# Optimization experiments

Measured on AMD Instinct MI355X. Metric: run time of the kernel, lower is better.

## Reference

```python
import jax, jax.numpy as jnp
from jax import lax
import numpy as np

# (pad, pool_kernel(h,w), pool_stride(h,w)) for each of the 7 conv layers
_CONV_CFG = [
    (1, (2, 2), (2, 2)),
    (1, (2, 2), (2, 2)),
    (1, (2, 2), (2, 1)),
    (1, (2, 2), (2, 1)),
    (1, (2, 2), (2, 2)),
    (1, (2, 2), (2, 1)),
    (0, (1, 1), (1, 1)),
]


def _conv_layer(x, w, b, pad, pool_k, pool_s):
    y = lax.conv_general_dilated(x, w, (1, 1), [(pad, pad), (pad, pad)],
                                 dimension_numbers=("NCHW", "OIHW", "NCHW"))
    y = jax.nn.relu(y + b[None, :, None, None])
    if pool_k != (1, 1):
        y = lax.reduce_window(y, -jnp.inf, lax.max, (1, 1) + pool_k, (1, 1) + pool_s, "VALID")
    return y


def _lstm_dir(x, wih, whh, bih, bhh, reverse):
    # x: [B,T,I]; PyTorch gate order i,f,g,o
    B = x.shape[0]
    H = whh.shape[1]
    xg = jnp.einsum("bti,gi->btg", x, wih) + bih + bhh  # [B,T,4H]

    def step(carry, xt):
        h, c = carry
        g = xt + h @ whh.T
        i, f, gg, o = jnp.split(g, 4, axis=-1)
        c = jax.nn.sigmoid(f) * c + jax.nn.sigmoid(i) * jnp.tanh(gg)
        h = jax.nn.sigmoid(o) * jnp.tanh(c)
        return (h, c), h

    init = (jnp.zeros((B, H), x.dtype), jnp.zeros((B, H), x.dtype))
    _, hs = lax.scan(step, init, jnp.swapaxes(xg, 0, 1), reverse=reverse)
    return jnp.swapaxes(hs, 0, 1)  # [B,T,H], time-ordered for both directions


def _bilstm2(x, wih, whh, bih, bhh, base):
    # 2-layer bidirectional LSTM; weight slots base..base+3 = (l0_fwd,l0_bwd,l1_fwd,l1_bwd)
    for l in range(2):
        i0 = base + 2 * l
        fwd = _lstm_dir(x, wih[i0], whh[i0], bih[i0], bhh[i0], False)
        bwd = _lstm_dir(x, wih[i0 + 1], whh[i0 + 1], bih[i0 + 1], bhh[i0 + 1], True)
        x = jnp.concatenate([fwd, bwd], axis=-1)
    return x


def _forward(x, conv_w0, conv_b0, conv_w1, conv_b1, conv_w2, conv_b2, conv_w3, conv_b3,
             conv_w4, conv_b4, conv_w5, conv_b5, conv_w6, conv_b6,
             lstm_wih, lstm_whh, lstm_bih, lstm_bhh,
             enc_proj_w, enc_proj_b, dec_proj_w, dec_proj_b, v_w,
             dec_wih, dec_whh, dec_bih, dec_bhh, dense_w, dense_b):
    conv_w = [conv_w0, conv_w1, conv_w2, conv_w3, conv_w4, conv_w5, conv_w6]
    conv_b = [conv_b0, conv_b1, conv_b2, conv_b3, conv_b4, conv_b5, conv_b6]
    y = x
    for i, (pad, pk, ps) in enumerate(_CONV_CFG):
        y = _conv_layer(y, conv_w[i], conv_b[i], pad, pk, ps)
    # y: [B,512,1,T] -> squeeze height, put time first-major: [B,T,512]
    y = jnp.transpose(y[:, :, 0, :], (0, 2, 1))
    seq = _bilstm2(y, lstm_wih, lstm_whh, lstm_bih, lstm_bhh, 0)
    seq = _bilstm2(seq, lstm_wih, lstm_whh, lstm_bih, lstm_bhh, 4)  # [B,T,512]

    # additive attention: enc projection is h-independent, precompute once
    enc = jnp.einsum("bte,ae->bta", seq, enc_proj_w) + enc_proj_b  # [B,T,256]
    B = x.shape[0]

    def dec_step(carry, _):
        h, c = carry
        dec = h @ dec_proj_w.T + dec_proj_b                      # [B,256]
        scores = jnp.tanh(enc + dec[:, None, :]) @ v_w[0]        # [B,T]
        aw = jax.nn.softmax(scores, axis=1)
        ctx = jnp.einsum("bt,bte->be", aw, seq)                  # [B,512]
        g = ctx @ dec_wih.T + dec_bih + h @ dec_whh.T + dec_bhh  # [B,2048]
        i, f, gg, o = jnp.split(g, 4, axis=-1)
        c = jax.nn.sigmoid(f) * c + jax.nn.sigmoid(i) * jnp.tanh(gg)
        h = jax.nn.sigmoid(o) * jnp.tanh(c)
        return (h, c), h @ dense_w.T + dense_b

    init = (jnp.zeros((B, 512), x.dtype), jnp.zeros((B, 512), x.dtype))
    _, outs = lax.scan(dec_step, init, None, length=25)  # [25,B,99] == permute(1,0,2)
    return outs


def setup_inputs() -> dict:
    key = jax.random.key(0)
    ks = jax.random.split(key, 32)

    def rn(i, shape, std):
        return jax.random.normal(ks[i], shape, jnp.float32) * std

    d = {"x": jax.random.normal(ks[0], (16, 1, 128, 512), jnp.float32)}
    chans = [(1, 64, 3), (64, 128, 3), (128, 256, 3), (256, 512, 3),
             (512, 512, 3), (512, 512, 3), (512, 512, 2)]
    for i, (ci, co, k) in enumerate(chans):
        d[f"conv_w{i}"] = rn(1 + i, (co, ci, k, k), (2.0 / (ci * k * k)) ** 0.5)
        d[f"conv_b{i}"] = rn(8 + i, (co,), 0.02)
    d["lstm_wih"] = rn(15, (8, 1024, 512), 0.06)
    d["lstm_whh"] = rn(16, (8, 1024, 256), 0.06)
    d["lstm_bih"] = rn(17, (8, 1024), 0.06)
    d["lstm_bhh"] = rn(18, (8, 1024), 0.06)
    d["enc_proj_w"] = rn(19, (256, 512), 0.04)
    d["enc_proj_b"] = rn(20, (256,), 0.02)
    d["dec_proj_w"] = rn(21, (256, 512), 0.04)
    d["dec_proj_b"] = rn(22, (256,), 0.02)
    d["v_w"] = rn(23, (1, 256), 0.06)
    d["dec_wih"] = rn(24, (2048, 512), 0.04)
    d["dec_whh"] = rn(25, (2048, 512), 0.04)
    d["dec_bih"] = rn(26, (2048,), 0.02)
    d["dec_bhh"] = rn(27, (2048,), 0.02)
    d["dense_w"] = rn(28, (99, 512), 0.04)
    d["dense_b"] = rn(29, (99,), 0.02)
    return d


def reference(x, conv_w0, conv_b0, conv_w1, conv_b1, conv_w2, conv_b2, conv_w3, conv_b3,
              conv_w4, conv_b4, conv_w5, conv_b5, conv_w6, conv_b6,
              lstm_wih, lstm_whh, lstm_bih, lstm_bhh,
              enc_proj_w, enc_proj_b, dec_proj_w, dec_proj_b, v_w,
              dec_wih, dec_whh, dec_bih, dec_bhh, dense_w, dense_b):
    return _forward(x, conv_w0, conv_b0, conv_w1, conv_b1, conv_w2, conv_b2, conv_w3, conv_b3,
                    conv_w4, conv_b4, conv_w5, conv_b5, conv_w6, conv_b6,
                    lstm_wih, lstm_whh, lstm_bih, lstm_bhh,
                    enc_proj_w, enc_proj_b, dec_proj_w, dec_proj_b, v_w,
                    dec_wih, dec_whh, dec_bih, dec_bhh, dense_w, dense_b)
```

## Files before the change

kernel.cpp:

```cpp
#include <hip/hip_runtime.h>
#include <math.h>

typedef short bf16x8 __attribute__((ext_vector_type(8)));
typedef short s16x4  __attribute__((ext_vector_type(4)));
typedef float f32x4  __attribute__((ext_vector_type(4)));

__device__ __forceinline__ float sigmf(float x){ return 1.f/(1.f+expf(-x)); }
__device__ __forceinline__ short f2bf(float f){
    unsigned u = __float_as_uint(f);
    u = (u + 0x7FFFu + ((u>>16)&1u)) >> 16;
    return (short)u;
}
__device__ __forceinline__ float bf2f(short s){
    return __uint_as_float(((unsigned)(unsigned short)s) << 16);
}

__global__ void wsplit(const float* __restrict__ w, short* __restrict__ whi, short* __restrict__ wlo,
                       int Cout, int Cin, int KW, int total)
{
    int idx = blockIdx.x*256 + threadIdx.x;
    if (idx >= total) return;
    int l = idx & 63; int t = idx >> 6;
    int KST = Cin >> 5;
    int ks = t % KST; t /= KST;
    int nCoQ = Cout >> 4;
    int coQ = t % nCoQ; int kk = t / nCoQ;
    int ky = kk / KW, kx = kk % KW;
    int co = coQ*16 + (l & 15);
    int ci = ks*32 + (l >> 4)*8;
    bf16x8 h, lo;
#pragma unroll
    for (int e = 0; e < 8; ++e) {
        float wv = w[(((size_t)co*Cin + ci + e)*KW + ky)*KW + kx];
        short hb = f2bf(wv);
        h[e] = hb;
        lo[e] = f2bf(wv - bf2f(hb));
    }
    ((bf16x8*)whi)[idx] = h;
    ((bf16x8*)wlo)[idx] = lo;
}

__global__ void wsplit_g(const float* __restrict__ w, short* __restrict__ out)
{
    int slot = blockIdx.y;
    int i = blockIdx.x*256 + threadIdx.x;
    int l = i & 63, t = i >> 6;
    int kc = t & 15, nQ = t >> 4;
    int n = nQ*16 + (l & 15);
    int k = kc*32 + (l >> 4)*8;
    const float* src = w + ((size_t)slot*1024 + n)*512 + k;
    bf16x8 h, lo;
#pragma unroll
    for (int e = 0; e < 8; ++e) {
        float wv = src[e];
        short hb = f2bf(wv);
        h[e] = hb;
        lo[e] = f2bf(wv - bf2f(hb));
    }
    short* o = out + (size_t)slot*1048576;
    ((bf16x8*)o)[i] = h;
    ((bf16x8*)(o + 524288))[i] = lo;
}

template<int KW, int PKH, int PKW, int PSW, int PAD, bool FUSE0>
__launch_bounds__(256)
__global__ void conv_mfma(const float* __restrict__ in, const short* __restrict__ wm,
                          const float* __restrict__ bias, float* __restrict__ out,
                          int Cin, int H, int W, int Cout, int Hp, int Wp, int Wel,
                          const float* __restrict__ w0, const float* __restrict__ b0)
{
    constexpr int TAPS = KW*KW;
    constexpr int SR   = PKH + KW - 1;
    constexpr int XT   = 64;
    constexpr int XTH  = 67;
    constexpr int POB  = (XT - PKW)/PSW + 1;
    __shared__ union {
        short s[2][16][XTH][8];
        float y[64][132];
    } u;
    __shared__ float w0s[640];

    const int tid  = threadIdx.x;
    const int lane = tid & 63;
    const int wid  = tid >> 6;
    const int l15  = lane & 15, l4 = lane >> 4;
    const int nCoT = Cout >> 7;
    const int b    = blockIdx.z / nCoT;
    const int ct   = blockIdx.z % nCoT;
    const int co_blk = ct << 7;
    const int hp   = blockIdx.y;
    const int px0  = blockIdx.x * POB;
    const int x0   = px0 * PSW;
    const int y0   = hp * PKH;
    const int cow  = wid >> 1;
    const int xw   = (wid & 1) * 32;
    const int KST  = Cin >> 5;
    const int nCoQ = Cout >> 4;

    if constexpr (FUSE0) {
        for (int i = tid; i < 640; i += 256) w0s[i] = (i < 576) ? w0[i] : b0[i-576];
    }

    f32x4 acc[4][2][PKH];
#pragma unroll
    for (int c = 0; c < 4; ++c)
#pragma unroll
        for (int xf = 0; xf < 2; ++xf)
#pragma unroll
            for (int r = 0; r < PKH; ++r) acc[c][xf][r] = (f32x4){0.f,0.f,0.f,0.f};

    const float* inb = FUSE0 ? (in + (size_t)b*128*512) : (in + (size_t)b*H*W*Cin);

    for (int ci0 = 0; ci0 < Cin; ci0 += 32) {
        __syncthreads();
        constexpr int ITEMS = SR*XTH*4;
        for (int it = tid; it < ITEMS; it += 256) {
            int kslot = it & 3;
            int x  = (it >> 2) % XTH;
            int r  = (it >> 2) / XTH;
            int y  = y0 - PAD + r;
            int xg = x0 - PAD + x;
            float v[8];
            if constexpr (FUSE0) {
                if (y >= 0 && y < H && xg >= 0 && xg < W) {
                    float xin[4][4];
                    int iy0 = 2*y - 1, ix0 = 2*xg - 1;
#pragma unroll
                    for (int dy = 0; dy < 4; ++dy) {
                        int iy = iy0 + dy;
                        bool oky = (iy >= 0) && (iy < 128);
#pragma unroll
                        for (int dx = 0; dx < 4; ++dx) {
                            int ix = ix0 + dx;
                            xin[dy][dx] = (oky && ix >= 0 && ix < 512) ? inb[(size_t)iy*512 + ix] : 0.f;
                        }
                    }
#pragma unroll
                    for (int c = 0; c < 8; ++c) {
                        int co = ci0 + kslot*8 + c;
                        const float* w9 = &w0s[co*9];
                        float p00=0.f,p01=0.f,p10=0.f,p11=0.f;
#pragma unroll
                        for (int ky = 0; ky < 3; ++ky)
#pragma unroll
                            for (int kx = 0; kx < 3; ++kx) {
                                float wv = w9[ky*3+kx];
                                p00 = fmaf(xin[ky  ][kx  ], wv, p00);
                                p01 = fmaf(xin[ky  ][kx+1], wv, p01);
                                p10 = fmaf(xin[ky+1][kx  ], wv, p10);
                                p11 = fmaf(xin[ky+1][kx+1], wv, p11);
                            }
                        float m = fmaxf(fmaxf(p00,p01), fmaxf(p10,p11)) + w0s[576+co];
                        v[c] = fmaxf(m, 0.f);
                    }
                } else {
#pragma unroll
                    for (int c = 0; c < 8; ++c) v[c] = 0.f;
                }
            } else {
                if (y >= 0 && y < H && xg >= 0 && xg < W) {
                    const float* p = inb + ((size_t)y*W + xg)*Cin + ci0 + kslot*8;
                    float4 a = *(const float4*)p;
                    float4 bq = *(const float4*)(p+4);
                    v[0]=a.x; v[1]=a.y; v[2]=a.z; v[3]=a.w;
                    v[4]=bq.x; v[5]=bq.y; v[6]=bq.z; v[7]=bq.w;
                } else {
#pragma unroll
                    for (int c = 0; c < 8; ++c) v[c] = 0.f;
                }
            }
            bf16x8 h8, l8;
#pragma unroll
            for (int c = 0; c < 8; ++c) {
                short hb = f2bf(v[c]);
                h8[c] = hb;
                l8[c] = f2bf(v[c] - bf2f(hb));
            }
            *(bf16x8*)&u.s[0][r*4+kslot][x][0] = h8;
            *(bf16x8*)&u.s[1][r*4+kslot][x][0] = l8;
        }
        __syncthreads();

        const int ks = ci0 >> 5;
        for (int kk = 0; kk < TAPS; ++kk) {
            const int ky = kk / KW, kx = kk % KW;
            bf16x8 ah[4], al[4];
            const size_t abase = (((size_t)kk*nCoQ + (co_blk>>4) + cow*4)*KST + ks)*512 + lane*8;
            const size_t cstr  = (size_t)KST*512;
#pragma unroll
            for (int c = 0; c < 4; ++c) {
                ah[c] = *(const bf16x8*)(wm + abase + c*cstr);
                al[c] = *(const bf16x8*)(wm + Wel + abase + c*cstr);
            }
#pragma unroll
            for (int r = 0; r < PKH; ++r) {
                const int sr = r + ky;
                bf16x8 bh[2], bl[2];
#pragma unroll
                for (int xf = 0; xf < 2; ++xf) {
                    int xcol = xw + xf*16 + l15 + kx;
                    bh[xf] = *(const bf16x8*)&u.s[0][sr*4 + l4][xcol][0];
                    bl[xf] = *(const bf16x8*)&u.s[1][sr*4 + l4][xcol][0];
                }
#pragma unroll
                for (int c = 0; c < 4; ++c)
#pragma unroll
                    for (int xf = 0; xf < 2; ++xf) {
                        acc[c][xf][r] = __builtin_amdgcn_mfma_f32_16x16x32_bf16(ah[c], bh[xf], acc[c][xf][r], 0,0,0);
                        acc[c][xf][r] = __builtin_amdgcn_mfma_f32_16x16x32_bf16(ah[c], bl[xf], acc[c][xf][r], 0,0,0);
                        acc[c][xf][r] = __builtin_amdgcn_mfma_f32_16x16x32_bf16(al[c], bh[xf], acc[c][xf][r], 0,0,0);
                    }
            }
        }
    }

    __syncthreads();
#pragma unroll
    for (int c = 0; c < 4; ++c) {
        int co_l = cow*64 + c*16 + l4*4;
        float4 b4 = *(const float4*)&bias[co_blk + co_l];
#pragma unroll
        for (int xf = 0; xf < 2; ++xf) {
            f32x4 v = acc[c][xf][0];
            if (PKH == 2) {
                f32x4 v1 = acc[c][xf][1];
                v[0]=fmaxf(v[0],v1[0]); v[1]=fmaxf(v[1],v1[1]);
                v[2]=fmaxf(v[2],v1[2]); v[3]=fmaxf(v[3],v1[3]);
            }
            v[0]+=b4.x; v[1]+=b4.y; v[2]+=b4.z; v[3]+=b4.w;
            int x = xw + xf*16 + l15;
            *(f32x4*)&u.y[x][co_l] = v;
        }
    }
    __syncthreads();
    for (int i = tid; i < POB*128; i += 256) {
        int co = i & 127, p = i >> 7;
        int x = p * PSW;
        float v = u.y[x][co];
        if (PKW == 2) v = fmaxf(v, u.y[x+1][co]);
        v = fmaxf(v, 0.f);
        int px = px0 + p;
        if (px < Wp)
            out[(((size_t)b*Hp + hp)*Wp + px)*Cout + co_blk + co] = v;
    }
}

__launch_bounds__(256)
__global__ void gemm_mfma(const float* __restrict__ A, const short* __restrict__ wg,
                          const float* __restrict__ bi, const float* __restrict__ bh,
                          float* __restrict__ Cf, float* __restrict__ Cb,
                          int M, int s0)
{
    __shared__ short sa[2][4][64][8];
    const int tid = threadIdx.x;
    const int lane = tid & 63;
    const int wid = tid >> 6;
    const int l15 = lane & 15, l4 = lane >> 4;
    const int cow = wid >> 1;
    const int xw  = wid & 1;
    const int m0 = blockIdx.x * 64;
    const int n0 = blockIdx.y * 128;
    const int slot = s0 + blockIdx.z;
    const short* whi = wg + (size_t)slot * 1048576;
    const short* wlo = whi + 524288;
    float* C = blockIdx.z ? Cb : Cf;
    const float* b1 = bi + slot*1024;
    const float* b2 = bh + slot*1024;

    const int mg  = wid;
    const int pos = tid & 63;
    const int sm  = mg*16 + (pos & 15);
    const int skl = pos >> 4;
    const int gm  = m0 + sm;
    const int nQb = blockIdx.y*8 + cow*4;

    f32x4 acc[4][2];
#pragma unroll
    for (int c = 0; c < 4; ++c)
#pragma unroll
        for (int xf = 0; xf < 2; ++xf) acc[c][xf] = (f32x4){0.f,0.f,0.f,0.f};

    for (int kc = 0; kc < 16; ++kc) {
        __syncthreads();
        {
            float v[8];
            if (gm < M) {
                const float* ap = A + (size_t)gm*512 + kc*32 + skl*8;
                float4 q0 = *(const float4*)ap;
                float4 q1 = *(const float4*)(ap+4);
                v[0]=q0.x; v[1]=q0.y; v[2]=q0.z; v[3]=q0.w;
                v[4]=q1.x; v[5]=q1.y; v[6]=q1.z; v[7]=q1.w;
            } else {
#pragma unroll
                for (int e = 0; e < 8; ++e) v[e] = 0.f;
            }
            bf16x8 h8, l8;
#pragma unroll
            for (int e = 0; e < 8; ++e) {
                short hb = f2bf(v[e]);
                h8[e] = hb;
                l8[e] = f2bf(v[e] - bf2f(hb));
            }
            *(bf16x8*)&sa[0][mg][pos][0] = h8;
            *(bf16x8*)&sa[1][mg][pos][0] = l8;
        }
        __syncthreads();

        bf16x8 ah[4], al[4];
#pragma unroll
        for (int c = 0; c < 4; ++c) {
            size_t off = (((size_t)(nQb + c)*16 + kc)*64 + lane)*8;
            ah[c] = *(const bf16x8*)(whi + off);
            al[c] = *(const bf16x8*)(wlo + off);
        }
        bf16x8 bhv[2], blv[2];
#pragma unroll
        for (int xf = 0; xf < 2; ++xf) {
            bhv[xf] = *(const bf16x8*)&sa[0][xw*2+xf][lane][0];
            blv[xf] = *(const bf16x8*)&sa[1][xw*2+xf][lane][0];
        }
#pragma unroll
        for (int c = 0; c < 4; ++c)
#pragma unroll
            for (int xf = 0; xf < 2; ++xf) {
                acc[c][xf] = __builtin_amdgcn_mfma_f32_16x16x32_bf16(ah[c], bhv[xf], acc[c][xf], 0,0,0);
                acc[c][xf] = __builtin_amdgcn_mfma_f32_16x16x32_bf16(ah[c], blv[xf], acc[c][xf], 0,0,0);
                acc[c][xf] = __builtin_amdgcn_mfma_f32_16x16x32_bf16(al[c], bhv[xf], acc[c][xf], 0,0,0);
            }
    }

#pragma unroll
    for (int c = 0; c < 4; ++c) {
        int n = n0 + cow*64 + c*16 + l4*4;
        float4 bb1 = *(const float4*)&b1[n];
        float4 bb2 = *(const float4*)&b2[n];
#pragma unroll
        for (int xf = 0; xf < 2; ++xf) {
            int m = m0 + xw*32 + xf*16 + l15;
            if (m < M) {
                f32x4 a = acc[c][xf];
                float4 o;
                o.x = a[0] + bb1.x + bb2.x;
                o.y = a[1] + bb1.y + bb2.y;
                o.z = a[2] + bb1.z + bb2.z;
                o.w = a[3] + bb1.w + bb2.w;
                *(float4*)&C[(size_t)m*1024 + n] = o;
            }
        }
    }
}

__launch_bounds__(256)
__global__ void gemm_nt(const float* __restrict__ A, const float* __restrict__ Bm,
                        const float* __restrict__ bias1, const float* __restrict__ bias2,
                        float* __restrict__ C, int M, int N, int K)
{
    __shared__ float As[16][68];
    __shared__ float Bs[16][68];
    const int tid = threadIdx.x;
    const int tx = tid & 15, ty = tid >> 4;
    const int row0 = blockIdx.y*64, col0 = blockIdx.x*64;
    float acc[4][4] = {};
    for (int k0 = 0; k0 < K; k0 += 16) {
#pragma unroll
        for (int i = 0; i < 4; ++i) {
            int e  = tid + i*256;
            int r  = e >> 4, kk = e & 15;
            int gr = row0 + r, gk = k0 + kk;
            As[kk][r] = (gr < M) ? A[(size_t)gr*K + gk] : 0.f;
            int gc = col0 + r;
            Bs[kk][r] = (gc < N) ? Bm[(size_t)gc*K + gk] : 0.f;
        }
        __syncthreads();
#pragma unroll
        for (int kk = 0; kk < 16; ++kk) {
            float av[4], bv[4];
#pragma unroll
            for (int i=0;i<4;++i) av[i] = As[kk][ty*4+i];
#pragma unroll
            for (int j=0;j<4;++j) bv[j] = Bs[kk][tx*4+j];
#pragma unroll
            for (int i=0;i<4;++i)
#pragma unroll
                for (int j=0;j<4;++j) acc[i][j] = fmaf(av[i], bv[j], acc[i][j]);
        }
        __syncthreads();
    }
#pragma unroll
    for (int i=0;i<4;++i)
#pragma unroll
        for (int j=0;j<4;++j) {
            int r = row0 + ty*4 + i, cc = col0 + tx*4 + j;
            if (r < M && cc < N) {
                float v = acc[i][j];
                if (bias1) v += bias1[cc];
                if (bias2) v += bias2[cc];
                C[(size_t)r*N + cc] = v;
            }
        }
}

__global__ void transpose2d(const float* __restrict__ in, float* __restrict__ out, int R, int C)
{
    int idx = blockIdx.x*256 + threadIdx.x;
    if (idx >= R*C) return;
    int r = idx / C, c = idx % C;
    out[(size_t)c*R + r] = in[idx];
}

__global__ void pack_whh_bf16(const float* __restrict__ in, short* __restrict__ out)
{
    int idx = blockIdx.x*256 + threadIdx.x;
    if (idx >= 8*1024*256) return;
    int l = idx / 262144, rem = idx % 262144;
    int g = rem >> 8, k = rem & 255;
    int j = g & 255, gate = g >> 8;
    out[(size_t)l*262144 + ((size_t)k*256 + j)*4 + gate] = f2bf(in[idx]);
}

__global__ void transpose_w4(const float* __restrict__ in, float* __restrict__ out)
{
    int idx = blockIdx.x*256 + threadIdx.x;
    if (idx >= 2048*512) return;
    int row = idx >> 9, k = idx & 511;
    int gate = row >> 9, j = row & 511;
    out[((size_t)k*512 + j)*4 + gate] = in[idx];
}

__launch_bounds__(1024)
__global__ void lstm_scan3(const float* __restrict__ xgf, const float* __restrict__ xgb,
                           const short* __restrict__ wBf, const short* __restrict__ wBb,
                           float* __restrict__ hout, int T)
{
    __shared__ float hs[256];
    __shared__ float part[4][256][4];
    const int b = blockIdx.x, dir = blockIdx.y;
    const int tid = threadIdx.x;
    const int j = tid & 255, ks = tid >> 8;
    const float* xg = dir ? xgb : xgf;
    const s16x4* w4 = (const s16x4*)(dir ? wBb : wBf);
    float c = 0.f;
    if (ks == 0) hs[j] = 0.f;
    __syncthreads();
    float* outp = hout + dir*256 + j;
    for (int s = 0; s < T; ++s) {
        int t = dir ? (T-1-s) : s;
        float xi=0.f, xf_=0.f, xg_=0.f, xo=0.f;
        if (ks == 0) {
            const float* xr = xg + ((size_t)b*T + t)*1024;
            xi = xr[j]; xf_ = xr[256+j]; xg_ = xr[512+j]; xo = xr[768+j];
        }
        float a0=0.f,a1=0.f,a2=0.f,a3=0.f;
        const s16x4* wp = w4 + (size_t)(ks*64)*256 + j;
#pragma unroll 16
        for (int kk = 0; kk < 64; ++kk) {
            float hv = hs[ks*64 + kk];
            s16x4 w = wp[(size_t)kk*256];
            a0 = fmaf(hv, bf2f(w[0]), a0);
            a1 = fmaf(hv, bf2f(w[1]), a1);
            a2 = fmaf(hv, bf2f(w[2]), a2);
            a3 = fmaf(hv, bf2f(w[3]), a3);
        }
        part[ks][j][0]=a0; part[ks][j][1]=a1; part[ks][j][2]=a2; part[ks][j][3]=a3;
        __syncthreads();
        if (ks == 0) {
            float gi = xi  + part[0][j][0]+part[1][j][0]+part[2][j][0]+part[3][j][0];
            float gf = xf_ + part[0][j][1]+part[1][j][1]+part[2][j][1]+part[3][j][1];
            float gg = xg_ + part[0][j][2]+part[1][j][2]+part[2][j][2]+part[3][j][2];
            float go = xo  + part[0][j][3]+part[1][j][3]+part[2][j][3]+part[3][j][3];
            c = sigmf(gf)*c + sigmf(gi)*tanhf(gg);
            float h = sigmf(go)*tanhf(c);
            hs[j] = h;
            outp[((size_t)b*T + t)*512] = h;
        }
        __syncthreads();
    }
}

__global__ void zero_hc(float* __restrict__ h, float* __restrict__ c)
{
    int i = blockIdx.x*256 + threadIdx.x;
    if (i < 16*512) { h[i] = 0.f; c[i] = 0.f; }
}

__launch_bounds__(256)
__global__ void dec_att(const float* __restrict__ h, const float* __restrict__ seq,
                        const float* __restrict__ enc, const float* __restrict__ dpwT,
                        const float* __restrict__ dpb, const float* __restrict__ vw,
                        float* __restrict__ ctx, int T)
{
    __shared__ float hsm[512], dec[256], sc[64];
    const int b = blockIdx.x, tid = threadIdx.x;
    hsm[tid]     = h[b*512 + tid];
    hsm[256+tid] = h[b*512 + 256 + tid];
    __syncthreads();
    float s = dpb[tid];
    for (int k = 0; k < 512; ++k) s = fmaf(hsm[k], dpwT[(size_t)k*256 + tid], s);
    dec[tid] = s;
    __syncthreads();
    {
        int t = tid >> 2, sub = tid & 3;
        float p = 0.f;
        if (t < T) {
            const float* er = enc + ((size_t)b*T + t)*256 + sub*64;
            const float* dc = dec + sub*64;
            const float* vv = vw + sub*64;
            for (int a = 0; a < 64; ++a) p = fmaf(tanhf(er[a] + dc[a]), vv[a], p);
        }
        p += __shfl_xor(p, 1, 4); p += __shfl_xor(p, 2, 4);
        if (t < T && sub == 0) sc[t] = p;
    }
    __syncthreads();
    if (tid < 64) {
        float v = (tid < T) ? sc[tid] : -1e30f;
        float m = v;
        for (int o = 1; o < 64; o <<= 1) m = fmaxf(m, __shfl_xor(m, o, 64));
        float e = (tid < T) ? expf(v - m) : 0.f;
        float ssum = e;
        for (int o = 1; o < 64; o <<= 1) ssum += __shfl_xor(ssum, o, 64);
        if (tid < T) sc[tid] = e / ssum;
    }
    __syncthreads();
#pragma unroll
    for (int half = 0; half < 2; ++half) {
        int col = tid + half*256;
        float acc = 0.f;
        const float* sr = seq + (size_t)b*T*512 + col;
        for (int t = 0; t < T; ++t) acc = fmaf(sc[t], sr[(size_t)t*512], acc);
        ctx[b*512 + col] = acc;
    }
}

__launch_bounds__(256)
__global__ void gates_part(const float* __restrict__ ctx, const float* __restrict__ h,
                           const float* __restrict__ wi4, const float* __restrict__ wh4,
                           float* __restrict__ gpart)
{
    __shared__ float xs[16][128], hsh[16][128];
    const int jt = blockIdx.x, ks = blockIdx.y;
    const int tid = threadIdx.x;
    const int jl = tid & 127, bh = tid >> 7;
    const int j = jt*128 + jl;
    const int k0 = ks*128;
    for (int idx = tid; idx < 2048; idx += 256) {
        int bb = idx >> 7, kk = idx & 127;
        xs[bb][kk]  = ctx[bb*512 + k0 + kk];
        hsh[bb][kk] = h[bb*512 + k0 + kk];
    }
    __syncthreads();
    float acc[8][4];
#pragma unroll
    for (int bi=0;bi<8;++bi)
#pragma unroll
        for (int g=0;g<4;++g) acc[bi][g]=0.f;
    const float4* wip = (const float4*)wi4 + (size_t)k0*512 + j;
    const float4* whp = (const float4*)wh4 + (size_t)k0*512 + j;
#pragma unroll 2
    for (int kk = 0; kk < 128; ++kk) {
        float4 wa = wip[(size_t)kk*512];
        float4 wb = whp[(size_t)kk*512];
#pragma unroll
        for (int bi = 0; bi < 8; ++bi) {
            int bb = bh*8 + bi;
            float xv = xs[bb][kk], hv = hsh[bb][kk];
            acc[bi][0] = fmaf(xv, wa.x, fmaf(hv, wb.x, acc[bi][0]));
            acc[bi][1] = fmaf(xv, wa.y, fmaf(hv, wb.y, acc[bi][1]));
            acc[bi][2] = fmaf(xv, wa.z, fmaf(hv, wb.z, acc[bi][2]));
            acc[bi][3] = fmaf(xv, wa.w, fmaf(hv, wb.w, acc[bi][3]));
        }
    }
    float* gp = gpart + (size_t)ks*16*2048;
#pragma unroll
    for (int bi = 0; bi < 8; ++bi)
#pragma unroll
        for (int g = 0; g < 4; ++g)
            gp[(size_t)(bh*8+bi)*2048 + j*4 + g] = acc[bi][g];
}

__launch_bounds__(512)
__global__ void cell_dense(float* __restrict__ h, float* __restrict__ c,
                           const float* __restrict__ gpart,
                           const float* __restrict__ bih, const float* __restrict__ bhh,
                           const float* __restrict__ dwT, const float* __restrict__ dnb,
                           float* __restrict__ out)
{
    __shared__ float hsh[512];
    const int b = blockIdx.x, j = threadIdx.x;
    float gi = bih[j]        + bhh[j];
    float gf = bih[512+j]    + bhh[512+j];
    float gg = bih[1024+j]   + bhh[1024+j];
    float go = bih[1536+j]   + bhh[1536+j];
#pragma unroll
    for (int ks = 0; ks < 4; ++ks) {
        float4 gp = *(const float4*)(gpart + (size_t)ks*16*2048 + (size_t)b*2048 + j*4);
        gi += gp.x; gf += gp.y; gg += gp.z; go += gp.w;
    }
    float cn = sigmf(gf)*c[b*512+j] + sigmf(gi)*tanhf(gg);
    float hn = sigmf(go)*tanhf(cn);
    c[b*512+j] = cn; h[b*512+j] = hn; hsh[j] = hn;
    __syncthreads();
    int o = j >> 2, sub = j & 3;
    float p = 0.f;
    if (o < 99) {
        const float* hk = hsh + sub*128;
        const float* wk = dwT + (size_t)sub*128*99 + o;
        for (int k = 0; k < 128; ++k) p = fmaf(hk[k], wk[(size_t)k*99], p);
    }
    p += __shfl_xor(p, 1, 4); p += __shfl_xor(p, 2, 4);
    if (o < 99 && sub == 0) out[b*99 + o] = p + dnb[o];
}

extern "C" void kernel_launch(void* const* d_in, const int* in_sizes, int n_in,
                              void* d_out, int out_size, void* d_ws, size_t ws_size,
                              hipStream_t stream)
{
    (void)in_sizes; (void)n_in; (void)out_size; (void)ws_size;
    const float* x = (const float*)d_in[0];
    const float* convw[7]; const float* convb[7];
    for (int i = 0; i < 7; ++i) { convw[i] = (const float*)d_in[1+2*i]; convb[i] = (const float*)d_in[2+2*i]; }
    const float* lw   = (const float*)d_in[15];
    const float* lr   = (const float*)d_in[16];
    const float* lbi  = (const float*)d_in[17];
    const float* lbh  = (const float*)d_in[18];
    const float* encW = (const float*)d_in[19];
    const float* encB = (const float*)d_in[20];
    const float* dpw  = (const float*)d_in[21];
    const float* dpb  = (const float*)d_in[22];
    const float* vw   = (const float*)d_in[23];
    const float* dwih = (const float*)d_in[24];
    const float* dwhh = (const float*)d_in[25];
    const float* dbih = (const float*)d_in[26];
    const float* dbhh = (const float*)d_in[27];
    const float* dnw  = (const float*)d_in[28];
    const float* dnb  = (const float*)d_in[29];
    float* outp = (float*)d_out;

    float* ws    = (float*)d_ws;
    float* bufA  = ws;
    float* bufB  = ws + 8388608;
    float* wscr  = ws + 16777216;
    float* S0    = ws + 19136512;
    float* SY    = ws + 19636224;
    float* xg_f  = ws + 20135936;
    float* xg_b  = ws + 21135360;
    float* whhBf = ws + 22134784;
    float* encb  = ws + 24231936;
    float* dpwT  = ws + 24481792;
    float* dwT   = ws + 24612864;
    float* hbuf  = ws + 24663552;
    float* cbuf  = ws + 24671744;
    float* ctxb  = ws + 24679936;
    float* gpart = ws + 24688128;
    float* wihT4 = bufA;
    float* whh2T4= bufB;
    short* wgB   = (short*)(bufA + 1048576);
    short* whhB  = (short*)whhBf;

    short* whi = (short*)wscr;

    {
        int Wel = 9*(128/16)*(64/32)*512;
        wsplit<<<(Wel/8+255)/256, 256, 0, stream>>>(convw[1], whi, whi+Wel, 128, 64, 3, Wel/8);
        conv_mfma<3,2,2,2,1,true><<<dim3(4,32,16), 256, 0, stream>>>(
            x, whi, convb[1], bufA, 64,64,256,128, 32,128, Wel, convw[0], convb[0]);
    }
    {
        int Wel = 9*(256/16)*(128/32)*512;
        wsplit<<<(Wel/8+255)/256, 256, 0, stream>>>(convw[2], whi, whi+Wel, 256, 128, 3, Wel/8);
        conv_mfma<3,2,2,1,1,false><<<dim3(3,16,32), 256, 0, stream>>>(
            bufA, whi, convb[2], bufB, 128,32,128,256, 16,127, Wel, nullptr, nullptr);
    }
    {
        int Wel = 9*(512/16)*(256/32)*512;
        wsplit<<<(Wel/8+255)/256, 256, 0, stream>>>(convw[3], whi, whi+Wel, 512, 256, 3, Wel/8);
        conv_mfma<3,2,2,1,1,false><<<dim3(2,8,64), 256, 0, stream>>>(
            bufB, whi, convb[3], bufA, 256,16,127,512, 8,126, Wel, nullptr, nullptr);
    }
    {
        int Wel = 9*(512/16)*(512/32)*512;
        wsplit<<<(Wel/8+255)/256, 256, 0, stream>>>(convw[4], whi, whi+Wel, 512, 512, 3, Wel/8);
        conv_mfma<3,2,2,2,1,false><<<dim3(2,4,64), 256, 0, stream>>>(
            bufA, whi, convb[4], bufB, 512,8,126,512, 4,63, Wel, nullptr, nullptr);
    }
    {
        int Wel = 9*(512/16)*(512/32)*512;
        wsplit<<<(Wel/8+255)/256, 256, 0, stream>>>(convw[5], whi, whi+Wel, 512, 512, 3, Wel/8);
        conv_mfma<3,2,2,1,1,false><<<dim3(1,2,64), 256, 0, stream>>>(
            bufB, whi, convb[5], bufA, 512,4,63,512, 2,62, Wel, nullptr, nullptr);
    }
    {
        int Wel = 4*(512/16)*(512/32)*512;
        wsplit<<<(Wel/8+255)/256, 256, 0, stream>>>(convw[6], whi, whi+Wel, 512, 512, 2, Wel/8);
        conv_mfma<2,1,1,1,0,false><<<dim3(1,1,64), 256, 0, stream>>>(
            bufA, whi, convb[6], S0, 512,2,62,512, 1,61, Wel, nullptr, nullptr);
    }

    wsplit_g<<<dim3(256, 8), 256, 0, stream>>>(lw, wgB);
    pack_whh_bf16<<<(8*1024*256 + 255)/256, 256, 0, stream>>>(lr, whhB);
    transpose2d<<<(256*512 + 255)/256, 256, 0, stream>>>(dpw, dpwT, 256, 512);
    transpose_w4<<<(2048*512 + 255)/256, 256, 0, stream>>>(dwih, wihT4);
    transpose_w4<<<(2048*512 + 255)/256, 256, 0, stream>>>(dwhh, whh2T4);
    transpose2d<<<(99*512 + 255)/256, 256, 0, stream>>>(dnw, dwT, 99, 512);

    const int T = 61, M = 16*T;
    float* cur = S0; float* nxt = SY;
    for (int L = 0; L < 4; ++L) {
        int s0 = 2*L;
        gemm_mfma<<<dim3(16, 8, 2), 256, 0, stream>>>(cur, wgB, lbi, lbh, xg_f, xg_b, M, s0);
        lstm_scan3<<<dim3(16,2), 1024, 0, stream>>>(xg_f, xg_b,
            whhB + (size_t)s0*262144, whhB + (size_t)(s0+1)*262144, nxt, T);
        float* tmp = cur; cur = nxt; nxt = tmp;
    }

    gemm_nt<<<dim3(4, (M+63)/64), 256, 0, stream>>>(cur, encW, encB, nullptr, encb, M, 256, 512);

    zero_hc<<<32, 256, 0, stream>>>(hbuf, cbuf);
    for (int step = 0; step < 25; ++step) {
        dec_att<<<16, 256, 0, stream>>>(hbuf, cur, encb, dpwT, dpb, vw, ctxb, T);
        gates_part<<<dim3(4,4), 256, 0, stream>>>(ctxb, hbuf, wihT4, whh2T4, gpart);
        cell_dense<<<16, 512, 0, stream>>>(hbuf, cbuf, gpart, dbih, dbhh, dwT, dnb,
                                           outp + (size_t)step*16*99);
    }
}
```

Before: 5.081 ms.

## Split LSTM recurrence across blocks with LDS-resident weights and flag-based sync

```diff
diff --git a/kernel.cpp b/kernel.cpp
--- a/kernel.cpp
+++ b/kernel.cpp
@@ -2,7 +2,6 @@
 #include <math.h>
 
 typedef short bf16x8 __attribute__((ext_vector_type(8)));
-typedef short s16x4  __attribute__((ext_vector_type(4)));
 typedef float f32x4  __attribute__((ext_vector_type(4)));
 
 __device__ __forceinline__ float sigmf(float x){ return 1.f/(1.f+expf(-x)); }
@@ -408,16 +407,6 @@
     out[(size_t)c*R + r] = in[idx];
 }
 
-__global__ void pack_whh_bf16(const float* __restrict__ in, short* __restrict__ out)
-{
-    int idx = blockIdx.x*256 + threadIdx.x;
-    if (idx >= 8*1024*256) return;
-    int l = idx / 262144, rem = idx % 262144;
-    int g = rem >> 8, k = rem & 255;
-    int j = g & 255, gate = g >> 8;
-    out[(size_t)l*262144 + ((size_t)k*256 + j)*4 + gate] = f2bf(in[idx]);
-}
-
 __global__ void transpose_w4(const float* __restrict__ in, float* __restrict__ out)
 {
     int idx = blockIdx.x*256 + threadIdx.x;
@@ -427,53 +416,104 @@
     out[((size_t)k*512 + j)*4 + gate] = in[idx];
 }
 
-__launch_bounds__(1024)
-__global__ void lstm_scan3(const float* __restrict__ xgf, const float* __restrict__ xgb,
-                           const short* __restrict__ wBf, const short* __restrict__ wBb,
-                           float* __restrict__ hout, int T)
-{
-    __shared__ float hs[256];
-    __shared__ float part[4][256][4];
-    const int b = blockIdx.x, dir = blockIdx.y;
+__global__ void zero_flags(int* __restrict__ flags, int n)
+{
+    int i = blockIdx.x*256 + threadIdx.x;
+    if (i < n) flags[i] = 0;
+}
+
+__launch_bounds__(256)
+__global__ void lstm_spin(const float* __restrict__ xgf, const float* __restrict__ xgb,
+                          const float* __restrict__ whh, float* __restrict__ hout,
+                          float* __restrict__ hx, int* __restrict__ flags,
+                          int T, int s0)
+{
+    __shared__ float wlds[32768];
+    __shared__ float hcur[1024];
+    __shared__ float parts[4096];
     const int tid = threadIdx.x;
-    const int j = tid & 255, ks = tid >> 8;
+    const int jq = blockIdx.x, bg = blockIdx.y, dir = blockIdx.z;
+    const int j0 = jq*32, b0 = bg*4;
+    const float* W = whh + (size_t)(s0 + dir)*262144;
+
+    for (int idx = tid; idx < 32768; idx += 256) {
+        int k = idx & 255, r = idx >> 8;
+        int jl = r & 31, g = r >> 5;
+        wlds[(k*32 + jl)*4 + g] = W[((size_t)g*256 + j0 + jl)*256 + k];
+    }
     const float* xg = dir ? xgb : xgf;
-    const s16x4* w4 = (const s16x4*)(dir ? wBb : wBf);
-    float c = 0.f;
-    if (ks == 0) hs[j] = 0.f;
-    __syncthreads();
-    float* outp = hout + dir*256 + j;
+    float* hxg = hx + (size_t)(dir*4 + bg)*2048;
+    int* flg = flags + (dir*4 + bg)*61;
+    const int jl_c = tid & 31, b_c = tid >> 5;
+    const int ks = tid >> 5, jl = tid & 31;
+    float cc = 0.f;
+    __syncthreads();
+
     for (int s = 0; s < T; ++s) {
-        int t = dir ? (T-1-s) : s;
-        float xi=0.f, xf_=0.f, xg_=0.f, xo=0.f;
-        if (ks == 0) {
-            const float* xr = xg + ((size_t)b*T + t)*1024;
-            xi = xr[j]; xf_ = xr[256+j]; xg_ = xr[512+j]; xo = xr[768+j];
-        }
-        float a0=0.f,a1=0.f,a2=0.f,a3=0.f;
-        const s16x4* wp = w4 + (size_t)(ks*64)*256 + j;
-#pragma unroll 16
-        for (int kk = 0; kk < 64; ++kk) {
-            float hv = hs[ks*64 + kk];
-            s16x4 w = wp[(size_t)kk*256];
-            a0 = fmaf(hv, bf2f(w[0]), a0);
-            a1 = fmaf(hv, bf2f(w[1]), a1);
-            a2 = fmaf(hv, bf2f(w[2]), a2);
-            a3 = fmaf(hv, bf2f(w[3]), a3);
-        }
-        part[ks][j][0]=a0; part[ks][j][1]=a1; part[ks][j][2]=a2; part[ks][j][3]=a3;
-        __syncthreads();
-        if (ks == 0) {
-            float gi = xi  + part[0][j][0]+part[1][j][0]+part[2][j][0]+part[3][j][0];
-            float gf = xf_ + part[0][j][1]+part[1][j][1]+part[2][j][1]+part[3][j][1];
-            float gg = xg_ + part[0][j][2]+part[1][j][2]+part[2][j][2]+part[3][j][2];
-            float go = xo  + part[0][j][3]+part[1][j][3]+part[2][j][3]+part[3][j][3];
-            c = sigmf(gf)*c + sigmf(gi)*tanhf(gg);
-            float h = sigmf(go)*tanhf(c);
-            hs[j] = h;
-            outp[((size_t)b*T + t)*512] = h;
-        }
-        __syncthreads();
+        const int t = dir ? (T-1-s) : s;
+        float xgv0=0.f, xgv1=0.f, xgv2=0.f, xgv3=0.f;
+        if (tid < 128) {
+            const float* xr = xg + ((size_t)(b0 + b_c)*T + t)*1024 + (j0 + jl_c);
+            xgv0 = xr[0]; xgv1 = xr[256]; xgv2 = xr[512]; xgv3 = xr[768];
+        }
+        if (s == 0) {
+            for (int i = tid; i < 1024; i += 256) hcur[i] = 0.f;
+        } else {
+            int* fp = flg + (s-1);
+            while (__hip_atomic_load(fp, __ATOMIC_ACQUIRE, __HIP_MEMORY_SCOPE_AGENT) < 8)
+                __builtin_amdgcn_s_sleep(1);
+            const float* hsrc = hxg + ((s-1)&1)*1024 + tid*4;
+            float v0 = __hip_atomic_load(hsrc+0, __ATOMIC_RELAXED, __HIP_MEMORY_SCOPE_AGENT);
+            float v1 = __hip_atomic_load(hsrc+1, __ATOMIC_RELAXED, __HIP_MEMORY_SCOPE_AGENT);
+            float v2 = __hip_atomic_load(hsrc+2, __ATOMIC_RELAXED, __HIP_MEMORY_SCOPE_AGENT);
+            float v3 = __hip_atomic_load(hsrc+3, __ATOMIC_RELAXED, __HIP_MEMORY_SCOPE_AGENT);
+            hcur[tid*4+0]=v0; hcur[tid*4+1]=v1; hcur[tid*4+2]=v2; hcur[tid*4+3]=v3;
+        }
+        __syncthreads();
+
+        float a[4][4];
+#pragma unroll
+        for (int g = 0; g < 4; ++g)
+#pragma unroll
+            for (int b = 0; b < 4; ++b) a[g][b] = 0.f;
+        for (int kk = 0; kk < 32; ++kk) {
+            int k = ks*32 + kk;
+            float4 wv = *(const float4*)&wlds[(k*32 + jl)*4];
+            float4 hv = *(const float4*)&hcur[k*4];
+            a[0][0] = fmaf(wv.x, hv.x, a[0][0]); a[0][1] = fmaf(wv.x, hv.y, a[0][1]);
+            a[0][2] = fmaf(wv.x, hv.z, a[0][2]); a[0][3] = fmaf(wv.x, hv.w, a[0][3]);
+            a[1][0] = fmaf(wv.y, hv.x, a[1][0]); a[1][1] = fmaf(wv.y, hv.y, a[1][1]);
+            a[1][2] = fmaf(wv.y, hv.z, a[1][2]); a[1][3] = fmaf(wv.y, hv.w, a[1][3]);
+            a[2][0] = fmaf(wv.z, hv.x, a[2][0]); a[2][1] = fmaf(wv.z, hv.y, a[2][1]);
+            a[2][2] = fmaf(wv.z, hv.z, a[2][2]); a[2][3] = fmaf(wv.z, hv.w, a[2][3]);
+            a[3][0] = fmaf(wv.w, hv.x, a[3][0]); a[3][1] = fmaf(wv.w, hv.y, a[3][1]);
+            a[3][2] = fmaf(wv.w, hv.z, a[3][2]); a[3][3] = fmaf(wv.w, hv.w, a[3][3]);
+        }
+#pragma unroll
+        for (int g = 0; g < 4; ++g)
+#pragma unroll
+            for (int b = 0; b < 4; ++b)
+                parts[((g*4 + b)*8 + ks)*32 + jl] = a[g][b];
+        __syncthreads();
+
+        if (tid < 128) {
+            float gi = xgv0, gf = xgv1, gg = xgv2, go = xgv3;
+#pragma unroll
+            for (int k2 = 0; k2 < 8; ++k2) {
+                gi += parts[((0*4 + b_c)*8 + k2)*32 + jl_c];
+                gf += parts[((1*4 + b_c)*8 + k2)*32 + jl_c];
+                gg += parts[((2*4 + b_c)*8 + k2)*32 + jl_c];
+                go += parts[((3*4 + b_c)*8 + k2)*32 + jl_c];
+            }
+            cc = sigmf(gf)*cc + sigmf(gi)*tanhf(gg);
+            float h = sigmf(go)*tanhf(cc);
+            hout[((size_t)(b0 + b_c)*T + t)*512 + dir*256 + j0 + jl_c] = h;
+            __hip_atomic_store(hxg + (s&1)*1024 + (j0 + jl_c)*4 + b_c, h,
+                               __ATOMIC_RELAXED, __HIP_MEMORY_SCOPE_AGENT);
+        }
+        __syncthreads();
+        if (tid == 0)
+            __hip_atomic_fetch_add(flg + s, 1, __ATOMIC_RELEASE, __HIP_MEMORY_SCOPE_AGENT);
     }
 }
 
@@ -643,7 +683,7 @@
     float* SY    = ws + 19636224;
     float* xg_f  = ws + 20135936;
     float* xg_b  = ws + 21135360;
-    float* whhBf = ws + 22134784;
+    float* hxfl  = ws + 22134784;
     float* encb  = ws + 24231936;
     float* dpwT  = ws + 24481792;
     float* dwT   = ws + 24612864;
@@ -654,7 +694,8 @@
     float* wihT4 = bufA;
     float* whh2T4= bufB;
     short* wgB   = (short*)(bufA + 1048576);
-    short* whhB  = (short*)whhBf;
+    float* hx    = hxfl;
+    int*   flags = (int*)(hxfl + 16384);
 
     short* whi = (short*)wscr;
 
@@ -696,7 +737,7 @@
     }
 
     wsplit_g<<<dim3(256, 8), 256, 0, stream>>>(lw, wgB);
-    pack_whh_bf16<<<(8*1024*256 + 255)/256, 256, 0, stream>>>(lr, whhB);
+    zero_flags<<<8, 256, 0, stream>>>(flags, 4*2*4*61);
     transpose2d<<<(256*512 + 255)/256, 256, 0, stream>>>(dpw, dpwT, 256, 512);
     transpose_w4<<<(2048*512 + 255)/256, 256, 0, stream>>>(dwih, wihT4);
     transpose_w4<<<(2048*512 + 255)/256, 256, 0, stream>>>(dwhh, whh2T4);
@@ -707,8 +748,8 @@
     for (int L = 0; L < 4; ++L) {
         int s0 = 2*L;
         gemm_mfma<<<dim3(16, 8, 2), 256, 0, stream>>>(cur, wgB, lbi, lbh, xg_f, xg_b, M, s0);
-        lstm_scan3<<<dim3(16,2), 1024, 0, stream>>>(xg_f, xg_b,
-            whhB + (size_t)s0*262144, whhB + (size_t)(s0+1)*262144, nxt, T);
+        lstm_spin<<<dim3(8, 4, 2), 256, 0, stream>>>(xg_f, xg_b, lr, nxt,
+                                                     hx, flags + L*488, T, s0);
         float* tmp = cur; cur = nxt; nxt = tmp;
     }
 
```

Result: faster. 4.708 ms (-7.3%).
